# Kernel tuning notes

Hardware: AMD Instinct MI355X
Metric: run time of the kernel (lower is better)

The kernel has to match this reference:

```python
import jax, jax.numpy as jnp
import numpy as np

EMBED_DIM = 768
NUM_HEADS = 12
HEAD_DIM = EMBED_DIM // NUM_HEADS
LN_EPS = 1e-5


def setup_inputs() -> dict:
    key = jax.random.key(0)
    ks = jax.random.split(key, 10)
    D = EMBED_DIM
    s = 1.0 / np.sqrt(D)
    x = jax.random.normal(ks[0], (2, 4096, D), dtype=jnp.float32)
    # nn.Linear weights stored as [out, in]; we keep [in, out] for x @ W.
    Wq = jax.random.uniform(ks[1], (D, D), jnp.float32, -s, s)
    bq = jax.random.uniform(ks[2], (D,), jnp.float32, -s, s)
    Wk = jax.random.uniform(ks[3], (D, D), jnp.float32, -s, s)
    bk = jax.random.uniform(ks[4], (D,), jnp.float32, -s, s)
    Wv = jax.random.uniform(ks[5], (D, D), jnp.float32, -s, s)
    bv = jax.random.uniform(ks[6], (D,), jnp.float32, -s, s)
    Wo = jax.random.uniform(ks[7], (D, D), jnp.float32, -s, s)
    bo = jax.random.uniform(ks[8], (D,), jnp.float32, -s, s)
    ln_g = jnp.ones((D,), jnp.float32)
    ln_b = jnp.zeros((D,), jnp.float32)
    return {"x": x, "Wq": Wq, "bq": bq, "Wk": Wk, "bk": bk,
            "Wv": Wv, "bv": bv, "Wo": Wo, "bo": bo,
            "ln_g": ln_g, "ln_b": ln_b}


def layer_norm(x, g, b):
    mu = jnp.mean(x, axis=-1, keepdims=True)
    var = jnp.mean(jnp.square(x - mu), axis=-1, keepdims=True)
    return (x - mu) * jax.lax.rsqrt(var + LN_EPS) * g + b


def reference(x, Wq, bq, Wk, bk, Wv, bv, Wo, bo, ln_g, ln_b):
    B, S, D = x.shape
    H, Hd = NUM_HEADS, HEAD_DIM
    residual = x
    xn = layer_norm(x, ln_g, ln_b)
    # [B,S,D] -> [B,H,S,Hd]
    def heads(t):
        return t.reshape(B, S, H, Hd).transpose(0, 2, 1, 3)
    q = heads(xn @ Wq + bq)
    k = heads(xn @ Wk + bk)
    v = heads(xn @ Wv + bv)
    scores = jnp.einsum('bhqd,bhkd->bhqk', q, k) / np.sqrt(Hd).astype(np.float32)
    attn = jax.nn.softmax(scores, axis=-1)  # dropout is identity in eval
    out = jnp.einsum('bhqk,bhkd->bhqd', attn, v)
    out = out.transpose(0, 2, 1, 3).reshape(B, S, D)
    out = out @ Wo + bo
    return out + residual
```

## Files before the change

### kernel.cpp

```cpp
#include <hip/hip_runtime.h>
#include <hip/hip_bf16.h>
#include <math.h>

constexpr int Bz = 2, Sq = 4096, Dm = 768, Hn = 12, Hd = 64;
constexpr int Mrows = Bz * Sq;
constexpr int LDQKV = 2304;

typedef short bf16x8 __attribute__((ext_vector_type(8)));
typedef short s16x4 __attribute__((ext_vector_type(4)));
typedef float f32x4 __attribute__((ext_vector_type(4)));

__device__ __forceinline__ short f2bf(float f) {
  unsigned u = __builtin_bit_cast(unsigned, f);
  u += 0x7fffu + ((u >> 16) & 1u);
  return (short)(u >> 16);
}

__device__ __forceinline__ unsigned cvt_pk_bf16(float a, float b) {
  unsigned r;
  asm("v_cvt_pk_bf16_f32 %0, %1, %2" : "=v"(r) : "v"(a), "v"(b));
  return r;
}

__global__ __launch_bounds__(256) void wprep_kernel(
    const float* __restrict__ Wq, const float* __restrict__ Wk,
    const float* __restrict__ Wv, const float* __restrict__ Wo,
    short* __restrict__ Wt) {
  __shared__ short T[64][72];
  const float* W = blockIdx.z == 0 ? Wq : blockIdx.z == 1 ? Wk
                 : blockIdx.z == 2 ? Wv : Wo;
  const int k0 = blockIdx.x * 64, n0 = blockIdx.y * 64;
  const int t = threadIdx.x;
  const int c4 = (t & 15) * 4, r = t >> 4;
#pragma unroll
  for (int i = 0; i < 4; ++i) {
    const int k = r + i * 16;
    const float4 wv = *(const float4*)(W + (size_t)(k0 + k) * 768 + n0 + c4);
    T[c4 + 0][k] = f2bf(wv.x);
    T[c4 + 1][k] = f2bf(wv.y);
    T[c4 + 2][k] = f2bf(wv.z);
    T[c4 + 3][k] = f2bf(wv.w);
  }
  __syncthreads();
  const int cn = t & 7, nn = t >> 3;
#pragma unroll
  for (int i = 0; i < 2; ++i) {
    const int n = nn + i * 32;
    *(bf16x8*)(Wt + ((size_t)blockIdx.z * 768 + n0 + n) * 768 + k0 + cn * 8) =
        *(const bf16x8*)&T[n][cn * 8];
  }
}

__global__ __launch_bounds__(256) void biaspack_kernel(
    const float* __restrict__ bq, const float* __restrict__ bk,
    const float* __restrict__ bv, const float* __restrict__ bo,
    float* __restrict__ dst) {
  const int j = blockIdx.x * 256 + threadIdx.x;
  dst[j] = j < 768 ? bq[j] : j < 1536 ? bk[j - 768]
         : j < 2304 ? bv[j - 1536] : bo[j - 2304];
}

__global__ __launch_bounds__(256) void ln_kernel(
    const float* __restrict__ x, const float* __restrict__ g,
    const float* __restrict__ b, short* __restrict__ xn) {
  const int row = blockIdx.x;
  const int t = threadIdx.x;
  const float* xr = x + (size_t)row * Dm;
  const float v0 = xr[t], v1 = xr[t + 256], v2 = xr[t + 512];
  float s = v0 + v1 + v2;
  float ss = v0 * v0 + v1 * v1 + v2 * v2;
#pragma unroll
  for (int m = 32; m >= 1; m >>= 1) {
    s += __shfl_xor(s, m);
    ss += __shfl_xor(ss, m);
  }
  __shared__ float red[8];
  const int wid = t >> 6, lane = t & 63;
  if (lane == 0) { red[wid] = s; red[4 + wid] = ss; }
  __syncthreads();
  s = red[0] + red[1] + red[2] + red[3];
  ss = red[4] + red[5] + red[6] + red[7];
  const float mu = s * (1.0f / Dm);
  const float var = ss * (1.0f / Dm) - mu * mu;
  const float rstd = rsqrtf(var + 1e-5f);
  short* xo = xn + (size_t)row * Dm;
  xo[t]       = f2bf((v0 - mu) * rstd * g[t]       + b[t]);
  xo[t + 256] = f2bf((v1 - mu) * rstd * g[t + 256] + b[t + 256]);
  xo[t + 512] = f2bf((v2 - mu) * rstd * g[t + 512] + b[t + 512]);
}

template <bool OUT_BF16, bool RESID, bool VTFUSE>
__global__ __launch_bounds__(256) void gemm128_kernel(
    const short* __restrict__ A, int ldA, const short* __restrict__ Bt,
    const float* __restrict__ bias, const float* __restrict__ resid,
    void* __restrict__ C, int ldC, short* __restrict__ vtp) {
  __shared__ short As[128 * 64];
  __shared__ short Bs[128 * 64];
  const int m0 = blockIdx.x * 128, n0 = blockIdx.y * 128;
  const int t = threadIdx.x;
  const int w = t >> 6, l = t & 63;
  const int wm = w >> 1, wn = w & 1;
  const int lr = l & 15, lg = l >> 4;
  const int srow = t >> 3, sslot = t & 7;

  f32x4 acc[4][4] = {};

  for (int kt = 0; kt < 768; kt += 64) {
    bf16x8 av[4], bv[4];
#pragma unroll
    for (int it = 0; it < 4; ++it) {
      const int row = it * 32 + srow;
      av[it] = *(const bf16x8*)(A + (size_t)(m0 + row) * ldA + kt + sslot * 8);
      bv[it] = *(const bf16x8*)(Bt + (size_t)(n0 + row) * 768 + kt + sslot * 8);
    }
    __syncthreads();
#pragma unroll
    for (int it = 0; it < 4; ++it) {
      const int row = it * 32 + srow;
      const int sidx = row * 64 + ((sslot ^ (row & 7)) * 8);
      *(bf16x8*)&As[sidx] = av[it];
      *(bf16x8*)&Bs[sidx] = bv[it];
    }
    __syncthreads();
#pragma unroll
    for (int ks = 0; ks < 2; ++ks) {
      bf16x8 af[4], bfr[4];
#pragma unroll
      for (int f = 0; f < 4; ++f) {
        const int ar = wm * 64 + f * 16 + lr;
        af[f] = *(const bf16x8*)&As[ar * 64 + (((ks * 4 + lg) ^ (ar & 7)) * 8)];
        const int br = wn * 64 + f * 16 + lr;
        bfr[f] = *(const bf16x8*)&Bs[br * 64 + (((ks * 4 + lg) ^ (br & 7)) * 8)];
      }
      __builtin_amdgcn_s_setprio(1);
#pragma unroll
      for (int mf = 0; mf < 4; ++mf)
#pragma unroll
        for (int nf = 0; nf < 4; ++nf)
          acc[mf][nf] = __builtin_amdgcn_mfma_f32_16x16x32_bf16(
              af[mf], bfr[nf], acc[mf][nf], 0, 0, 0);
      __builtin_amdgcn_s_setprio(0);
    }
  }

  const int colbase = n0 + wn * 64;
  const int rowbase = m0 + wm * 64;
  const bool vpath = VTFUSE && (n0 >= 1536);
#pragma unroll
  for (int nf = 0; nf < 4; ++nf) {
    const int col = colbase + nf * 16 + lr;
    const float bb = bias[col];
    if (vpath) {
      const int dcol = col - 1536;
      const int hh = dcol >> 6, dd = dcol & 63;
#pragma unroll
      for (int mf = 0; mf < 4; ++mf) {
        const int row0_ = rowbase + mf * 16 + lg * 4;
        const int bI = row0_ >> 12;
        const int s0 = row0_ & 4095;
        s16x4 pk;
#pragma unroll
        for (int rr = 0; rr < 4; ++rr) pk[rr] = f2bf(acc[mf][nf][rr] + bb);
        *(s16x4*)(vtp + ((size_t)(bI * Hn + hh) * Hd + dd) * Sq + s0) = pk;
      }
    } else {
#pragma unroll
      for (int mf = 0; mf < 4; ++mf) {
#pragma unroll
        for (int rr = 0; rr < 4; ++rr) {
          const int row = rowbase + mf * 16 + lg * 4 + rr;
          const float vv = acc[mf][nf][rr] + bb;
          if constexpr (OUT_BF16) {
            ((short*)C)[(size_t)row * ldC + col] = f2bf(vv);
          } else {
            ((float*)C)[(size_t)row * ldC + col] =
                vv + resid[(size_t)row * 768 + col];
          }
        }
      }
    }
  }
}

__global__ __launch_bounds__(256) void attn_mfma_kernel(
    const short* __restrict__ qg, const short* __restrict__ kg,
    const short* __restrict__ vt, short* __restrict__ o) {
  __shared__ short Ks[64 * 64];
  __shared__ short Vs[64 * 64];
  __shared__ short Ps[4][16 * 64];
  const int q0 = blockIdx.x * 64;
  const int h = blockIdx.y, b = blockIdx.z;
  const size_t qkbase = ((size_t)b * Sq) * LDQKV + (size_t)h * Hd;
  const size_t vbase = ((size_t)(b * Hn + h) * Hd) * Sq;
  const size_t obase = ((size_t)b * Sq) * Dm + (size_t)h * Hd;
  const int t = threadIdx.x;
  const int w = t >> 6, l = t & 63;
  const int lr = l & 15, lg = l >> 4;

  bf16x8 aq0, aq1;
  {
    const short* qp = qg + qkbase + (size_t)(q0 + w * 16 + lr) * LDQKV + lg * 8;
    aq0 = *(const bf16x8*)qp;
    aq1 = *(const bf16x8*)(qp + 32);
  }

  float mrow = -INFINITY;
  float lrow = 0.f;
  f32x4 oacc[4] = {};

  constexpr float SC = 0.18033688011112042f;

  const int srow = t >> 3, sslot = t & 7;
  const int srow1 = srow + 32;

  bf16x8 kreg0 = *(const bf16x8*)(kg + qkbase + (size_t)srow * LDQKV + sslot * 8);
  bf16x8 kreg1 = *(const bf16x8*)(kg + qkbase + (size_t)srow1 * LDQKV + sslot * 8);
  bf16x8 vreg0 = *(const bf16x8*)(vt + vbase + (size_t)srow * Sq + sslot * 8);
  bf16x8 vreg1 = *(const bf16x8*)(vt + vbase + (size_t)srow1 * Sq + sslot * 8);

  for (int kt = 0; kt < Sq; kt += 64) {
    __syncthreads();
    *(bf16x8*)&Ks[srow * 64 + ((sslot ^ (srow & 7)) * 8)] = kreg0;
    *(bf16x8*)&Ks[srow1 * 64 + ((sslot ^ (srow1 & 7)) * 8)] = kreg1;
    *(bf16x8*)&Vs[srow * 64 + ((sslot ^ (srow & 7)) * 8)] = vreg0;
    *(bf16x8*)&Vs[srow1 * 64 + ((sslot ^ (srow1 & 7)) * 8)] = vreg1;
    __syncthreads();

    if (kt + 64 < Sq) {
      const int ktn = kt + 64;
      kreg0 = *(const bf16x8*)(kg + qkbase + (size_t)(ktn + srow) * LDQKV + sslot * 8);
      kreg1 = *(const bf16x8*)(kg + qkbase + (size_t)(ktn + srow1) * LDQKV + sslot * 8);
      vreg0 = *(const bf16x8*)(vt + vbase + (size_t)srow * Sq + ktn + sslot * 8);
      vreg1 = *(const bf16x8*)(vt + vbase + (size_t)srow1 * Sq + ktn + sslot * 8);
    }

    f32x4 s[4];
    __builtin_amdgcn_s_setprio(1);
#pragma unroll
    for (int nt = 0; nt < 4; ++nt) {
      const int jr = nt * 16 + lr;
      const bf16x8 k0 = *(const bf16x8*)&Ks[jr * 64 + ((lg ^ (jr & 7)) * 8)];
      const bf16x8 k1 = *(const bf16x8*)&Ks[jr * 64 + (((4 + lg) ^ (jr & 7)) * 8)];
      f32x4 acc = {};
      acc = __builtin_amdgcn_mfma_f32_16x16x32_bf16(k0, aq0, acc, 0, 0, 0);
      acc = __builtin_amdgcn_mfma_f32_16x16x32_bf16(k1, aq1, acc, 0, 0, 0);
      s[nt] = acc;
    }
    __builtin_amdgcn_s_setprio(0);

    const float a0 = fmaxf(fmaxf(s[0][0], s[0][1]), s[0][2]);
    const float a1 = fmaxf(fmaxf(s[0][3], s[1][0]), s[1][1]);
    const float a2 = fmaxf(fmaxf(s[1][2], s[1][3]), s[2][0]);
    const float a3 = fmaxf(fmaxf(s[2][1], s[2][2]), s[2][3]);
    const float a4 = fmaxf(fmaxf(s[3][0], s[3][1]), s[3][2]);
    float tm = fmaxf(fmaxf(fmaxf(a0, a1), fmaxf(a2, a3)), fmaxf(a4, s[3][3]));
    tm = fmaxf(tm, __shfl_xor(tm, 16));
    tm = fmaxf(tm, __shfl_xor(tm, 32));

    const float mn = fmaxf(mrow, tm * SC);
    const float esc = __builtin_amdgcn_exp2f(mrow - mn);
    mrow = mn;
    const float negmn = -mn;
    float psum = 0.f;
#pragma unroll
    for (int nt = 0; nt < 4; ++nt)
#pragma unroll
      for (int r = 0; r < 4; ++r) {
        const float p = __builtin_amdgcn_exp2f(fmaf(s[nt][r], SC, negmn));
        s[nt][r] = p;
        psum += p;
      }
    lrow = lrow * esc + psum;

    float escq[4];
#pragma unroll
    for (int r = 0; r < 4; ++r) escq[r] = __shfl(esc, lg * 4 + r);
#pragma unroll
    for (int nt = 0; nt < 4; ++nt)
#pragma unroll
      for (int r = 0; r < 4; ++r) oacc[nt][r] *= escq[r];

#pragma unroll
    for (int nt = 0; nt < 4; ++nt) {
      uint2 pk;
      pk.x = cvt_pk_bf16(s[nt][0], s[nt][1]);
      pk.y = cvt_pk_bf16(s[nt][2], s[nt][3]);
      const int slot = (nt * 2 + (lg >> 1)) ^ (lr & 7);
      *(uint2*)&Ps[w][lr * 64 + slot * 8 + (lg & 1) * 4] = pk;
    }
    const bf16x8 ap0 = *(const bf16x8*)&Ps[w][lr * 64 + ((lg ^ (lr & 7)) * 8)];
    const bf16x8 ap1 = *(const bf16x8*)&Ps[w][lr * 64 + (((4 + lg) ^ (lr & 7)) * 8)];

    __builtin_amdgcn_s_setprio(1);
#pragma unroll
    for (int nt = 0; nt < 4; ++nt) {
      const int dr = nt * 16 + lr;
      const bf16x8 b0 = *(const bf16x8*)&Vs[dr * 64 + ((lg ^ (dr & 7)) * 8)];
      const bf16x8 b1 = *(const bf16x8*)&Vs[dr * 64 + (((4 + lg) ^ (dr & 7)) * 8)];
      oacc[nt] = __builtin_amdgcn_mfma_f32_16x16x32_bf16(ap0, b0, oacc[nt], 0, 0, 0);
      oacc[nt] = __builtin_amdgcn_mfma_f32_16x16x32_bf16(ap1, b1, oacc[nt], 0, 0, 0);
    }
    __builtin_amdgcn_s_setprio(0);
  }

  float lt = lrow + __shfl_xor(lrow, 16);
  lt += __shfl_xor(lt, 32);
  const float inv = 1.0f / lt;
  float invq[4];
#pragma unroll
  for (int r = 0; r < 4; ++r) invq[r] = __shfl(inv, lg * 4 + r);
#pragma unroll
  for (int r = 0; r < 4; ++r) {
    short* orow = o + obase + (size_t)(q0 + w * 16 + lg * 4 + r) * Dm;
#pragma unroll
    for (int nt = 0; nt < 4; ++nt)
      orow[nt * 16 + lr] = f2bf(oacc[nt][r] * invq[r]);
  }
}

extern "C" void kernel_launch(void* const* d_in, const int* in_sizes, int n_in,
                              void* d_out, int out_size, void* d_ws, size_t ws_size,
                              hipStream_t stream) {
  (void)in_sizes; (void)n_in; (void)out_size; (void)ws_size;
  const float* x  = (const float*)d_in[0];
  const float* Wq = (const float*)d_in[1];
  const float* bq = (const float*)d_in[2];
  const float* Wk = (const float*)d_in[3];
  const float* bk = (const float*)d_in[4];
  const float* Wv = (const float*)d_in[5];
  const float* bv = (const float*)d_in[6];
  const float* Wo = (const float*)d_in[7];
  const float* bo = (const float*)d_in[8];
  const float* lg = (const float*)d_in[9];
  const float* lb = (const float*)d_in[10];
  float* out = (float*)d_out;

  const size_t n = (size_t)Mrows * Dm;
  short* ws16 = (short*)d_ws;
  short* xn   = ws16;
  short* qkv  = xn + n;
  short* vt   = qkv + (size_t)Mrows * LDQKV;
  short* ab   = vt + n;
  short* Wt   = ab + n;
  float* ball = (float*)(Wt + (size_t)3072 * 768);

  wprep_kernel<<<dim3(12, 12, 4), 256, 0, stream>>>(Wq, Wk, Wv, Wo, Wt);
  biaspack_kernel<<<12, 256, 0, stream>>>(bq, bk, bv, bo, ball);
  ln_kernel<<<Mrows, 256, 0, stream>>>(x, lg, lb, xn);
  gemm128_kernel<true, false, true><<<dim3(Mrows / 128, LDQKV / 128), 256, 0, stream>>>(
      xn, Dm, Wt, ball, nullptr, qkv, LDQKV, vt);
  attn_mfma_kernel<<<dim3(Sq / 64, Hn, Bz), 256, 0, stream>>>(qkv, qkv + 768, vt, ab);
  gemm128_kernel<false, true, false><<<dim3(Mrows / 128, Dm / 128), 256, 0, stream>>>(
      ab, Dm, Wt + (size_t)2304 * 768, ball + 2304, x, out, Dm, nullptr);
}
```

Measured before the change: 361.0 us.

## Use direct global-to-LDS loads in GEMM and double-buffered attention K/V staging

Replaces the register-staged global loads plus LDS stores in the GEMM and attention kernels with global_load_lds 16-byte direct-to-LDS transfers. The swizzle moves to the global address side. The attention kernel now double-buffers K/V tiles in LDS, issuing the next tile's loads before computing on the current one, and drops one barrier per iteration. This is meant to cut VGPR pressure and LDS write instructions and to overlap memory with compute. The cost is double the K/V LDS footprint, and the GEMM has no prefetch overlap since it syncs right after issuing its loads.

```diff
diff --git a/kernel.cpp b/kernel.cpp
--- a/kernel.cpp
+++ b/kernel.cpp
@@ -20,6 +20,12 @@
   unsigned r;
   asm("v_cvt_pk_bf16_f32 %0, %1, %2" : "=v"(r) : "v"(a), "v"(b));
   return r;
+}
+
+typedef const __attribute__((address_space(1))) void* gas_cvp;
+typedef __attribute__((address_space(3))) void* las_vp;
+__device__ __forceinline__ void gload_lds16(const void* g, void* l) {
+  __builtin_amdgcn_global_load_lds((gas_cvp)g, (las_vp)l, 16, 0, 0);
 }
 
 __global__ __launch_bounds__(256) void wprep_kernel(
@@ -101,25 +107,19 @@
   const int w = t >> 6, l = t & 63;
   const int wm = w >> 1, wn = w & 1;
   const int lr = l & 15, lg = l >> 4;
-  const int srow = t >> 3, sslot = t & 7;
+  const int rg = l >> 3, slot = l & 7;
 
   f32x4 acc[4][4] = {};
 
   for (int kt = 0; kt < 768; kt += 64) {
-    bf16x8 av[4], bv[4];
+    __syncthreads();
 #pragma unroll
     for (int it = 0; it < 4; ++it) {
-      const int row = it * 32 + srow;
-      av[it] = *(const bf16x8*)(A + (size_t)(m0 + row) * ldA + kt + sslot * 8);
-      bv[it] = *(const bf16x8*)(Bt + (size_t)(n0 + row) * 768 + kt + sslot * 8);
-    }
-    __syncthreads();
-#pragma unroll
-    for (int it = 0; it < 4; ++it) {
-      const int row = it * 32 + srow;
-      const int sidx = row * 64 + ((sslot ^ (row & 7)) * 8);
-      *(bf16x8*)&As[sidx] = av[it];
-      *(bf16x8*)&Bs[sidx] = bv[it];
+      const int rowb = it * 32 + w * 8;
+      const int row = rowb + rg;
+      const int kc = kt + ((slot ^ rg) * 8);
+      gload_lds16(A + (size_t)(m0 + row) * ldA + kc, &As[rowb * 64]);
+      gload_lds16(Bt + (size_t)(n0 + row) * 768 + kc, &Bs[rowb * 64]);
     }
     __syncthreads();
 #pragma unroll
@@ -185,8 +185,8 @@
 __global__ __launch_bounds__(256) void attn_mfma_kernel(
     const short* __restrict__ qg, const short* __restrict__ kg,
     const short* __restrict__ vt, short* __restrict__ o) {
-  __shared__ short Ks[64 * 64];
-  __shared__ short Vs[64 * 64];
+  __shared__ short Ks[2][64 * 64];
+  __shared__ short Vs[2][64 * 64];
   __shared__ short Ps[4][16 * 64];
   const int q0 = blockIdx.x * 64;
   const int h = blockIdx.y, b = blockIdx.z;
@@ -196,6 +196,7 @@
   const int t = threadIdx.x;
   const int w = t >> 6, l = t & 63;
   const int lr = l & 15, lg = l >> 4;
+  const int rg = l >> 3, slot = l & 7;
 
   bf16x8 aq0, aq1;
   {
@@ -210,37 +211,33 @@
 
   constexpr float SC = 0.18033688011112042f;
 
-  const int srow = t >> 3, sslot = t & 7;
-  const int srow1 = srow + 32;
-
-  bf16x8 kreg0 = *(const bf16x8*)(kg + qkbase + (size_t)srow * LDQKV + sslot * 8);
-  bf16x8 kreg1 = *(const bf16x8*)(kg + qkbase + (size_t)srow1 * LDQKV + sslot * 8);
-  bf16x8 vreg0 = *(const bf16x8*)(vt + vbase + (size_t)srow * Sq + sslot * 8);
-  bf16x8 vreg1 = *(const bf16x8*)(vt + vbase + (size_t)srow1 * Sq + sslot * 8);
+  auto stage = [&](int buf, int kt) {
+#pragma unroll
+    for (int it = 0; it < 2; ++it) {
+      const int rowb = it * 32 + w * 8;
+      const int row = rowb + rg;
+      const int sc = (slot ^ rg) * 8;
+      gload_lds16(kg + qkbase + (size_t)(kt + row) * LDQKV + sc,
+                  &Ks[buf][rowb * 64]);
+      gload_lds16(vt + vbase + (size_t)row * Sq + kt + sc,
+                  &Vs[buf][rowb * 64]);
+    }
+  };
+
+  stage(0, 0);
+  __syncthreads();
+  int cur = 0;
 
   for (int kt = 0; kt < Sq; kt += 64) {
-    __syncthreads();
-    *(bf16x8*)&Ks[srow * 64 + ((sslot ^ (srow & 7)) * 8)] = kreg0;
-    *(bf16x8*)&Ks[srow1 * 64 + ((sslot ^ (srow1 & 7)) * 8)] = kreg1;
-    *(bf16x8*)&Vs[srow * 64 + ((sslot ^ (srow & 7)) * 8)] = vreg0;
-    *(bf16x8*)&Vs[srow1 * 64 + ((sslot ^ (srow1 & 7)) * 8)] = vreg1;
-    __syncthreads();
-
-    if (kt + 64 < Sq) {
-      const int ktn = kt + 64;
-      kreg0 = *(const bf16x8*)(kg + qkbase + (size_t)(ktn + srow) * LDQKV + sslot * 8);
-      kreg1 = *(const bf16x8*)(kg + qkbase + (size_t)(ktn + srow1) * LDQKV + sslot * 8);
-      vreg0 = *(const bf16x8*)(vt + vbase + (size_t)srow * Sq + ktn + sslot * 8);
-      vreg1 = *(const bf16x8*)(vt + vbase + (size_t)srow1 * Sq + ktn + sslot * 8);
-    }
+    if (kt + 64 < Sq) stage(cur ^ 1, kt + 64);
 
     f32x4 s[4];
     __builtin_amdgcn_s_setprio(1);
 #pragma unroll
     for (int nt = 0; nt < 4; ++nt) {
       const int jr = nt * 16 + lr;
-      const bf16x8 k0 = *(const bf16x8*)&Ks[jr * 64 + ((lg ^ (jr & 7)) * 8)];
-      const bf16x8 k1 = *(const bf16x8*)&Ks[jr * 64 + (((4 + lg) ^ (jr & 7)) * 8)];
+      const bf16x8 k0 = *(const bf16x8*)&Ks[cur][jr * 64 + ((lg ^ (jr & 7)) * 8)];
+      const bf16x8 k1 = *(const bf16x8*)&Ks[cur][jr * 64 + (((4 + lg) ^ (jr & 7)) * 8)];
       f32x4 acc = {};
       acc = __builtin_amdgcn_mfma_f32_16x16x32_bf16(k0, aq0, acc, 0, 0, 0);
       acc = __builtin_amdgcn_mfma_f32_16x16x32_bf16(k1, aq1, acc, 0, 0, 0);
@@ -285,8 +282,8 @@
       uint2 pk;
       pk.x = cvt_pk_bf16(s[nt][0], s[nt][1]);
       pk.y = cvt_pk_bf16(s[nt][2], s[nt][3]);
-      const int slot = (nt * 2 + (lg >> 1)) ^ (lr & 7);
-      *(uint2*)&Ps[w][lr * 64 + slot * 8 + (lg & 1) * 4] = pk;
+      const int pslot = (nt * 2 + (lg >> 1)) ^ (lr & 7);
+      *(uint2*)&Ps[w][lr * 64 + pslot * 8 + (lg & 1) * 4] = pk;
     }
     const bf16x8 ap0 = *(const bf16x8*)&Ps[w][lr * 64 + ((lg ^ (lr & 7)) * 8)];
     const bf16x8 ap1 = *(const bf16x8*)&Ps[w][lr * 64 + (((4 + lg) ^ (lr & 7)) * 8)];
@@ -295,12 +292,15 @@
 #pragma unroll
     for (int nt = 0; nt < 4; ++nt) {
       const int dr = nt * 16 + lr;
-      const bf16x8 b0 = *(const bf16x8*)&Vs[dr * 64 + ((lg ^ (dr & 7)) * 8)];
-      const bf16x8 b1 = *(const bf16x8*)&Vs[dr * 64 + (((4 + lg) ^ (dr & 7)) * 8)];
+      const bf16x8 b0 = *(const bf16x8*)&Vs[cur][dr * 64 + ((lg ^ (dr & 7)) * 8)];
+      const bf16x8 b1 = *(const bf16x8*)&Vs[cur][dr * 64 + (((4 + lg) ^ (dr & 7)) * 8)];
       oacc[nt] = __builtin_amdgcn_mfma_f32_16x16x32_bf16(ap0, b0, oacc[nt], 0, 0, 0);
       oacc[nt] = __builtin_amdgcn_mfma_f32_16x16x32_bf16(ap1, b1, oacc[nt], 0, 0, 0);
     }
     __builtin_amdgcn_s_setprio(0);
+
+    __syncthreads();
+    cur ^= 1;
   }
 
   float lt = lrow + __shfl_xor(lrow, 16);
```

New measurement: 369.9 us. 1.02x slower.

## Load GEMM tiles directly into LDS and skip rescaling on small max growth

Applied to the files above, without the earlier changes.

The GEMM mainloop now uses global_load_lds to copy A/B tiles straight from global memory into swizzled shared memory. This removes the register staging and the separate LDS store pass. The flash-attention loop also skips the running-max update and accumulator rescale unless some row's new max exceeds the old one by more than 8 in log2 scale. That saves the exp, shuffles and multiplies on most iterations, at the cost of letting exponentials grow up to 2^8 before renormalisation.

```diff
diff --git a/kernel.cpp b/kernel.cpp
--- a/kernel.cpp
+++ b/kernel.cpp
@@ -20,6 +20,12 @@
   unsigned r;
   asm("v_cvt_pk_bf16_f32 %0, %1, %2" : "=v"(r) : "v"(a), "v"(b));
   return r;
+}
+
+typedef const __attribute__((address_space(1))) void* gas_cvp;
+typedef __attribute__((address_space(3))) void* las_vp;
+__device__ __forceinline__ void gload_lds16(const void* g, void* l) {
+  __builtin_amdgcn_global_load_lds((gas_cvp)g, (las_vp)l, 16, 0, 0);
 }
 
 __global__ __launch_bounds__(256) void wprep_kernel(
@@ -101,25 +107,19 @@
   const int w = t >> 6, l = t & 63;
   const int wm = w >> 1, wn = w & 1;
   const int lr = l & 15, lg = l >> 4;
-  const int srow = t >> 3, sslot = t & 7;
+  const int rg = l >> 3, slot = l & 7;
 
   f32x4 acc[4][4] = {};
 
   for (int kt = 0; kt < 768; kt += 64) {
-    bf16x8 av[4], bv[4];
+    __syncthreads();
 #pragma unroll
     for (int it = 0; it < 4; ++it) {
-      const int row = it * 32 + srow;
-      av[it] = *(const bf16x8*)(A + (size_t)(m0 + row) * ldA + kt + sslot * 8);
-      bv[it] = *(const bf16x8*)(Bt + (size_t)(n0 + row) * 768 + kt + sslot * 8);
-    }
-    __syncthreads();
-#pragma unroll
-    for (int it = 0; it < 4; ++it) {
-      const int row = it * 32 + srow;
-      const int sidx = row * 64 + ((sslot ^ (row & 7)) * 8);
-      *(bf16x8*)&As[sidx] = av[it];
-      *(bf16x8*)&Bs[sidx] = bv[it];
+      const int rowb = it * 32 + w * 8;
+      const int row = rowb + rg;
+      const int kc = kt + ((slot ^ rg) * 8);
+      gload_lds16(A + (size_t)(m0 + row) * ldA + kc, &As[rowb * 64]);
+      gload_lds16(Bt + (size_t)(n0 + row) * 768 + kc, &Bs[rowb * 64]);
     }
     __syncthreads();
 #pragma unroll
@@ -256,11 +256,23 @@
     float tm = fmaxf(fmaxf(fmaxf(a0, a1), fmaxf(a2, a3)), fmaxf(a4, s[3][3]));
     tm = fmaxf(tm, __shfl_xor(tm, 16));
     tm = fmaxf(tm, __shfl_xor(tm, 32));
-
-    const float mn = fmaxf(mrow, tm * SC);
-    const float esc = __builtin_amdgcn_exp2f(mrow - mn);
-    mrow = mn;
-    const float negmn = -mn;
+    const float tms = tm * SC;
+
+    if (!__all(tms - mrow <= 8.0f)) {
+      const float mn = fmaxf(mrow, tms);
+      const float esc = __builtin_amdgcn_exp2f(mrow - mn);
+      mrow = mn;
+      lrow *= esc;
+      float escq[4];
+#pragma unroll
+      for (int r = 0; r < 4; ++r) escq[r] = __shfl(esc, lg * 4 + r);
+#pragma unroll
+      for (int nt = 0; nt < 4; ++nt)
+#pragma unroll
+        for (int r = 0; r < 4; ++r) oacc[nt][r] *= escq[r];
+    }
+
+    const float negmn = -mrow;
     float psum = 0.f;
 #pragma unroll
     for (int nt = 0; nt < 4; ++nt)
@@ -270,23 +282,15 @@
         s[nt][r] = p;
         psum += p;
       }
-    lrow = lrow * esc + psum;
-
-    float escq[4];
-#pragma unroll
-    for (int r = 0; r < 4; ++r) escq[r] = __shfl(esc, lg * 4 + r);
-#pragma unroll
-    for (int nt = 0; nt < 4; ++nt)
-#pragma unroll
-      for (int r = 0; r < 4; ++r) oacc[nt][r] *= escq[r];
+    lrow += psum;
 
 #pragma unroll
     for (int nt = 0; nt < 4; ++nt) {
       uint2 pk;
       pk.x = cvt_pk_bf16(s[nt][0], s[nt][1]);
       pk.y = cvt_pk_bf16(s[nt][2], s[nt][3]);
-      const int slot = (nt * 2 + (lg >> 1)) ^ (lr & 7);
-      *(uint2*)&Ps[w][lr * 64 + slot * 8 + (lg & 1) * 4] = pk;
+      const int pslot = (nt * 2 + (lg >> 1)) ^ (lr & 7);
+      *(uint2*)&Ps[w][lr * 64 + pslot * 8 + (lg & 1) * 4] = pk;
     }
     const bf16x8 ap0 = *(const bf16x8*)&Ps[w][lr * 64 + ((lg ^ (lr & 7)) * 8)];
     const bf16x8 ap1 = *(const bf16x8*)&Ps[w][lr * 64 + (((4 + lg) ^ (lr & 7)) * 8)];
```

New measurement: 355.5 us. Within noise of the previous version (-1.5%).
